# Optimization experiments

Hardware: AMD Instinct MI355X
Metric: run time of the kernel (lower is better)

The kernel has to match this reference:

```python
import jax, jax.numpy as jnp
import numpy as np

B, S, HID, NH = 2, 2048, 2048, 16
DH = HID // NH  # 128


def _rope_tables(seq_len, dim, dtype=jnp.float32):
    inv_freq = 1.0 / (10000.0 ** (jnp.arange(0, dim, 2, dtype=jnp.float32) / dim))
    t = jnp.arange(seq_len, dtype=jnp.float32)
    freqs = jnp.einsum('i,j->ij', t, inv_freq)          # [S, dim/2]
    emb = jnp.concatenate([freqs, freqs], axis=-1)       # [S, dim]
    return jnp.cos(emb)[None, None].astype(dtype), jnp.sin(emb)[None, None].astype(dtype)


def _rotate_half(x):
    x1, x2 = x[..., : x.shape[-1] // 2], x[..., x.shape[-1] // 2 :]
    return jnp.concatenate([-x2, x1], axis=-1)


def setup_inputs() -> dict:
    key = jax.random.key(0)
    ks = jax.random.split(key, 6)
    hidden_states = jax.random.normal(ks[0], (B, S, HID), dtype=jnp.float32)
    scale = 1.0 / np.sqrt(HID)
    Wq = jax.random.normal(ks[1], (HID, HID), dtype=jnp.float32) * scale
    Wk = jax.random.normal(ks[2], (HID, HID), dtype=jnp.float32) * scale
    Wv = jax.random.normal(ks[3], (HID, HID), dtype=jnp.float32) * scale
    Wo = jax.random.normal(ks[4], (HID, HID), dtype=jnp.float32) * scale
    bq = jnp.zeros((HID,), jnp.float32)
    bk = jnp.zeros((HID,), jnp.float32)
    bv = jnp.zeros((HID,), jnp.float32)
    bo = jnp.zeros((HID,), jnp.float32)
    # causal additive mask [1,1,S,S]
    causal = jnp.tril(jnp.ones((S, S), dtype=bool))
    attention_mask = jnp.where(causal, 0.0, -1e9).astype(jnp.float32)[None, None]
    return dict(hidden_states=hidden_states, attention_mask=attention_mask,
                Wq=Wq, bq=bq, Wk=Wk, bk=bk, Wv=Wv, bv=bv, Wo=Wo, bo=bo)


def reference(hidden_states, attention_mask, Wq, bq, Wk, bk, Wv, bv, Wo, bo):
    b, s, _ = hidden_states.shape
    # torch Linear: x @ W.T + b
    q = (hidden_states @ Wq.T + bq).reshape(b, s, NH, DH).transpose(0, 2, 1, 3)
    k = (hidden_states @ Wk.T + bk).reshape(b, s, NH, DH).transpose(0, 2, 1, 3)
    v = (hidden_states @ Wv.T + bv).reshape(b, s, NH, DH).transpose(0, 2, 1, 3)
    cos, sin = _rope_tables(s, DH)
    q = q * cos + _rotate_half(q) * sin
    k = k * cos + _rotate_half(k) * sin
    scores = jnp.einsum('bhqd,bhkd->bhqk', q * (DH ** -0.5), k)
    scores = scores + attention_mask
    probs = jax.nn.softmax(scores, axis=-1)  # dropout: eval mode (identity)
    out = jnp.einsum('bhqk,bhkd->bhqd', probs, v)
    out = out.transpose(0, 2, 1, 3).reshape(b, s, HID)
    return out @ Wo.T + bo
```

## Files before the change

### kernel.cpp

```cpp
#include <hip/hip_runtime.h>
#include <hip/hip_bf16.h>
#include <cstdint>
#include <cstddef>

#define BB 2
#define SS 2048
#define HH 2048
#define NHH 16
#define DHH 128

using f32x4  = __attribute__((ext_vector_type(4))) float;
using bf16x8 = __attribute__((ext_vector_type(8))) __bf16;
using bf16x4 = __attribute__((ext_vector_type(4))) __bf16;
using bfloat = __bf16;

__device__ inline void gload_lds16(const void* g, void* l) {
    __builtin_amdgcn_global_load_lds(
        (const __attribute__((address_space(1))) void*)g,
        (__attribute__((address_space(3))) void*)l, 16, 0, 0);
}

__device__ inline f32x4 mfma16(bf16x8 a, bf16x8 b, f32x4 c) {
    return __builtin_amdgcn_mfma_f32_16x16x32_bf16(a, b, c, 0, 0, 0);
}

template <int CTRL>
__device__ inline float dpp_max_step(float x) {
    int y = __builtin_amdgcn_update_dpp(0, __builtin_bit_cast(int, x), CTRL, 0xf, 0xf, false);
    return fmaxf(x, __builtin_bit_cast(float, y));
}
__device__ inline float rowmax16(float x) {
    x = dpp_max_step<0x121>(x);
    x = dpp_max_step<0x122>(x);
    x = dpp_max_step<0x124>(x);
    x = dpp_max_step<0x128>(x);
    return x;
}

__global__ void cvt_bf16(const float* __restrict__ in, bfloat* __restrict__ out, int n4) {
    int i = blockIdx.x * blockDim.x + threadIdx.x;
    if (i >= n4) return;
    float4 v = reinterpret_cast<const float4*>(in)[i];
    bf16x4 o;
    o[0] = (bfloat)v.x; o[1] = (bfloat)v.y; o[2] = (bfloat)v.z; o[3] = (bfloat)v.w;
    reinterpret_cast<bf16x4*>(out)[i] = o;
}

__global__ void cvt_bf16_w(const float* __restrict__ s0, const float* __restrict__ s1,
                           const float* __restrict__ s2, const float* __restrict__ s3,
                           bfloat* __restrict__ d0, bfloat* __restrict__ d1,
                           bfloat* __restrict__ d2, bfloat* __restrict__ d3) {
    int sel = blockIdx.x >> 12;
    int i = (blockIdx.x & 4095) * 256 + threadIdx.x;
    const float* s = sel == 0 ? s0 : sel == 1 ? s1 : sel == 2 ? s2 : s3;
    bfloat* d = sel == 0 ? d0 : sel == 1 ? d1 : sel == 2 ? d2 : d3;
    float4 v = reinterpret_cast<const float4*>(s)[i];
    bf16x4 o;
    o[0] = (bfloat)v.x; o[1] = (bfloat)v.y; o[2] = (bfloat)v.z; o[3] = (bfloat)v.w;
    reinterpret_cast<bf16x4*>(d)[i] = o;
}

__global__ void rope_table(float* __restrict__ cosT, float* __restrict__ sinT) {
    int i = blockIdx.x * blockDim.x + threadIdx.x;
    if (i >= SS * 64) return;
    int s = i >> 6, j = i & 63;
    float invf = powf(10000.0f, -(float)j / 64.0f);
    float ang = (float)s * invf;
    cosT[i] = cosf(ang);
    sinT[i] = sinf(ang);
}

__device__ __forceinline__ int cmap256(int wc, int nf) {
    return (wc >> 1) * 128 + (wc & 1) * 32 + (nf & 1) * 16 + (nf >> 1) * 64;
}

__device__ __forceinline__ void kloop256sq(const bfloat* __restrict__ Ag,
                                           const bfloat* __restrict__ Bg,
                                           f32x4 (&acc)[8][4]) {
    constexpr int K = HH, NT = K / 64;
    __shared__ bfloat Ab[2][256 * 64];
    __shared__ bfloat Bb[2][256 * 64];
    const int t = threadIdx.x, l = t & 63, lr = l & 15, lg = l >> 4;
    const int wid = t >> 6, wr = wid >> 2, wc = wid & 3;
    const int dstu = t & ~63;

    auto stage = [&](int buf, int kt) {
#pragma unroll
        for (int i = 0; i < 4; i++) {
            int U = i * 512 + t, row = U >> 3, u = (U & 7) ^ (row & 7);
            gload_lds16(Ag + (size_t)row * K + kt * 64 + u * 8,
                        &Ab[buf][(i * 512 + dstu) * 8]);
        }
#pragma unroll
        for (int i = 0; i < 4; i++) {
            int U = i * 512 + t, row = U >> 3, u = (U & 7) ^ (row & 7);
            gload_lds16(Bg + (size_t)row * K + kt * 64 + u * 8,
                        &Bb[buf][(i * 512 + dstu) * 8]);
        }
    };

    int brow[4];
#pragma unroll
    for (int nf = 0; nf < 4; nf++) brow[nf] = cmap256(wc, nf) + lr;
    const int usw[2] = { lg ^ (lr & 7), (4 + lg) ^ (lr & 7) };

    stage(0, 0);

#pragma unroll 1
    for (int kt = 0; kt < NT; ++kt) {
        const int buf = kt & 1;
        if (kt + 1 < NT) {
            stage(buf ^ 1, kt + 1);
            asm volatile("s_waitcnt vmcnt(8)" ::: "memory");
        } else {
            asm volatile("s_waitcnt vmcnt(0)" ::: "memory");
        }
        __builtin_amdgcn_s_barrier();
        __builtin_amdgcn_sched_barrier(0);

        const bfloat* A_ = Ab[buf];
        const bfloat* B_ = Bb[buf];
#pragma unroll
        for (int ks = 0; ks < 2; ++ks) {
            bf16x8 bfrag[4];
#pragma unroll
            for (int nf = 0; nf < 4; nf++)
                bfrag[nf] = *reinterpret_cast<const bf16x8*>(&B_[brow[nf] * 64 + usw[ks] * 8]);
            bf16x8 afr[4];
#pragma unroll
            for (int mf = 0; mf < 4; mf++)
                afr[mf] = *reinterpret_cast<const bf16x8*>(
                    &A_[(wr * 128 + mf * 16 + lr) * 64 + usw[ks] * 8]);
            __builtin_amdgcn_s_setprio(1);
#pragma unroll
            for (int mf = 0; mf < 4; mf++)
#pragma unroll
                for (int nf = 0; nf < 4; nf++)
                    acc[mf][nf] = mfma16(afr[mf], bfrag[nf], acc[mf][nf]);
            __builtin_amdgcn_s_setprio(0);
            __builtin_amdgcn_sched_barrier(0);
#pragma unroll
            for (int mf = 0; mf < 4; mf++)
                afr[mf] = *reinterpret_cast<const bf16x8*>(
                    &A_[(wr * 128 + (mf + 4) * 16 + lr) * 64 + usw[ks] * 8]);
            __builtin_amdgcn_s_setprio(1);
#pragma unroll
            for (int mf = 0; mf < 4; mf++)
#pragma unroll
                for (int nf = 0; nf < 4; nf++)
                    acc[mf + 4][nf] = mfma16(afr[mf], bfrag[nf], acc[mf + 4][nf]);
            __builtin_amdgcn_s_setprio(0);
            __builtin_amdgcn_sched_barrier(0);
        }
        __builtin_amdgcn_s_barrier();
    }
}

__global__ __launch_bounds__(512, 2)
void gemm_qkv(const bfloat* __restrict__ A,
              const bfloat* __restrict__ Bq, const bfloat* __restrict__ Bk,
              const bfloat* __restrict__ Bv,
              const float* __restrict__ bq, const float* __restrict__ bk,
              const float* __restrict__ bv,
              bfloat* __restrict__ Qo, bfloat* __restrict__ Ko, bfloat* __restrict__ Vto,
              const float* __restrict__ cosT, const float* __restrict__ sinT) {
    constexpr int K = HH, N = HH;
    const int sel = blockIdx.y >> 3;
    const bfloat* Bt = sel == 0 ? Bq : sel == 1 ? Bk : Bv;
    const float* bias = sel == 0 ? bq : sel == 1 ? bk : bv;
    const int m0 = blockIdx.x * 256, n0 = (blockIdx.y & 7) * 256;

    f32x4 acc[8][4] = {};
    kloop256sq(A + (size_t)m0 * K, Bt + (size_t)n0 * K, acc);

    const int t = threadIdx.x, l = t & 63, lr = l & 15, lg = l >> 4;
    const int wid = t >> 6, wr = wid >> 2, wc = wid & 3;

    if (sel == 2) {
#pragma unroll
        for (int mf = 0; mf < 8; mf++) {
            int row = m0 + wr * 128 + mf * 16 + lg * 4;
#pragma unroll
            for (int nf = 0; nf < 4; nf++) {
                int col = n0 + cmap256(wc, nf) + lr;
                float bv_ = bias[col];
#pragma unroll
                for (int j = 0; j < 4; j++) {
                    int r = row + j;
                    Vto[((size_t)((r >> 11) * HH + col)) * SS + (r & (SS - 1))] =
                        (bfloat)(acc[mf][nf][j] + bv_);
                }
            }
        }
    } else {
        bfloat* C = sel == 0 ? Qo : Ko;
        const float qs = sel == 0 ? 0.088388347648318447f : 1.0f;
        const int hbase = n0 + (wc >> 1) * 128;
#pragma unroll
        for (int mf = 0; mf < 8; mf++) {
            int row = m0 + wr * 128 + mf * 16 + lg * 4;
#pragma unroll
            for (int nf = 0; nf < 2; nf++) {
                int d = (wc & 1) * 32 + nf * 16 + lr;
                int col1 = hbase + d, col2 = col1 + 64;
                float b1 = bias[col1], b2 = bias[col2];
#pragma unroll
                for (int j = 0; j < 4; j++) {
                    int r = row + j, s = r & (SS - 1);
                    float c  = cosT[s * 64 + d];
                    float sn = sinT[s * 64 + d];
                    float x1 = acc[mf][nf][j] + b1;
                    float x2 = acc[mf][nf + 2][j] + b2;
                    C[(size_t)r * N + col1] = (bfloat)((x1 * c - x2 * sn) * qs);
                    C[(size_t)r * N + col2] = (bfloat)((x2 * c + x1 * sn) * qs);
                }
            }
        }
    }
}

__global__ __launch_bounds__(512, 2)
void gemm_out(const bfloat* __restrict__ A, const bfloat* __restrict__ Bt,
              const float* __restrict__ bias, float* __restrict__ C) {
    constexpr int K = HH, N = HH;
    const int m0 = blockIdx.x * 256, n0 = blockIdx.y * 256;

    f32x4 acc[8][4] = {};
    kloop256sq(A + (size_t)m0 * K, Bt + (size_t)n0 * K, acc);

    const int t = threadIdx.x, l = t & 63, lr = l & 15, lg = l >> 4;
    const int wid = t >> 6, wr = wid >> 2, wc = wid & 3;
#pragma unroll
    for (int mf = 0; mf < 8; mf++) {
        int row = m0 + wr * 128 + mf * 16 + lg * 4;
#pragma unroll
        for (int nf = 0; nf < 4; nf++) {
            int col = n0 + cmap256(wc, nf) + lr;
            float bv = bias[col];
#pragma unroll
            for (int j = 0; j < 4; j++)
                C[(size_t)(row + j) * N + col] = acc[mf][nf][j] + bv;
        }
    }
}

__global__ __launch_bounds__(256, 4)
void attn_fwd(const bfloat* __restrict__ Q, const bfloat* __restrict__ K,
              const bfloat* __restrict__ Vt, bfloat* __restrict__ O) {
    __shared__ bfloat Ks[64 * 128];
    __shared__ bfloat Vs[128 * 64];
    __shared__ bfloat Pw[4][16 * 64];

    const int t = threadIdx.x, w = t >> 6, l = t & 63;
    const int lr = l & 15, lg = l >> 4;
    const int swz = (lr & 7) << 4;

    const int f = blockIdx.x;
    const int xcd = f & 7, slot = f >> 3;
    const int bh = xcd + 8 * (slot >> 5);
    const int qidx = 31 - (slot & 31);
    const int b = bh >> 4, h = bh & 15;
    const int q0 = qidx * 64 + w * 16;

    const size_t bo_ = (size_t)b * SS * HH + (size_t)h * DHH;
    const bfloat* Qp = Q + bo_;
    const bfloat* Kp = K + bo_;
    const bfloat* Vp = Vt + (size_t)(b * NHH + h) * DHH * SS;
    bfloat* Op = O + bo_;

    auto stage = [&](int kv0) {
#pragma unroll
        for (int i = 0; i < 4; i++) {
            int Ub = (i * 4 + w) * 64;
            int U = Ub + l;
            int r = U >> 4;
            int u = (U & 15) ^ (r & 7);
            gload_lds16(Kp + (size_t)(kv0 + r) * HH + u * 8, &Ks[Ub * 8]);
        }
#pragma unroll
        for (int i = 0; i < 4; i++) {
            int Ub = (i * 4 + w) * 64;
            int U = Ub + l;
            int r = U >> 3;
            int u = (U & 7) ^ (r & 7);
            gload_lds16(Vp + (size_t)r * SS + kv0 + u * 8, &Vs[Ub * 8]);
        }
    };

    bf16x8 qf[4];
#pragma unroll
    for (int kt = 0; kt < 4; kt++)
        qf[kt] = *reinterpret_cast<const bf16x8*>(Qp + (size_t)(q0 + lr) * HH + kt * 32 + lg * 8);

    bf16x8 ones;
#pragma unroll
    for (int e = 0; e < 8; e++) ones[e] = (bfloat)1.0f;

    f32x4 o[8] = {};
    f32x4 lsv = {};
    float m[4];
#pragma unroll
    for (int j = 0; j < 4; j++) m[j] = -1e30f;

    const int nkv = qidx + 1;

    for (int kv = 0; kv < nkv; ++kv) {
        stage(kv * 64);
        __syncthreads();

        const char* KB = (const char*)&Ks[0];
        const char* VB = (const char*)&Vs[0];

        f32x4 sc[4] = {};
        __builtin_amdgcn_s_setprio(1);
#pragma unroll
        for (int kt = 0; kt < 4; kt++) {
            const int col = (kt * 64 + lg * 16);
#pragma unroll
            for (int kb = 0; kb < 4; kb++) {
                bf16x8 kf = *reinterpret_cast<const bf16x8*>(
                    KB + (kb * 16 + lr) * 256 + (col ^ swz));
                sc[kb] = mfma16(qf[kt], kf, sc[kb]);
            }
        }
        __builtin_amdgcn_s_setprio(0);

        const bool diag = (kv == nkv - 1);
        float p[4][4], alpha[4];
        bool ga = false;
#pragma unroll
        for (int j = 0; j < 4; j++) {
            float v0 = sc[0][j], v1 = sc[1][j], v2 = sc[2][j], v3 = sc[3][j];
            if (diag) {
                int qr = q0 + lg * 4 + j;
                int k0 = kv * 64 + lr;
                if (k0      > qr) v0 = -1e30f;
                if (k0 + 16 > qr) v1 = -1e30f;
                if (k0 + 32 > qr) v2 = -1e30f;
                if (k0 + 48 > qr) v3 = -1e30f;
            }
            float mx = rowmax16(fmaxf(fmaxf(v0, v1), fmaxf(v2, v3)));
            bool grow = mx > m[j] + 8.0f;
            float mn = grow ? mx : m[j];
            alpha[j] = grow ? __expf(m[j] - mn) : 1.0f;
            m[j] = mn;
            ga = ga || grow;
            p[0][j] = __expf(v0 - mn);
            p[1][j] = __expf(v1 - mn);
            p[2][j] = __expf(v2 - mn);
            p[3][j] = __expf(v3 - mn);
        }
        if (__any(ga)) {
#pragma unroll
            for (int j = 0; j < 4; j++) {
                lsv[j] *= alpha[j];
#pragma unroll
                for (int nt = 0; nt < 8; nt++) o[nt][j] *= alpha[j];
            }
        }

        char* pwb = (char*)&Pw[w][0];
#pragma unroll
        for (int j = 0; j < 4; j++) {
            int q = lg * 4 + j;
            int qs = (q & 7) << 4;
#pragma unroll
            for (int kb = 0; kb < 4; kb++)
                *(bfloat*)(pwb + q * 128 + ((kb * 32 + lr * 2) ^ qs)) = (bfloat)p[kb][j];
        }
        asm volatile("s_waitcnt lgkmcnt(0)" ::: "memory");
        __builtin_amdgcn_sched_barrier(0);

        const char* pwr = (const char*)&Pw[w][0];
        bf16x8 pa0 = *reinterpret_cast<const bf16x8*>(pwr + lr * 128 + ((lg * 16) ^ swz));
        bf16x8 pa1 = *reinterpret_cast<const bf16x8*>(pwr + lr * 128 + ((64 + lg * 16) ^ swz));
        __builtin_amdgcn_s_setprio(1);
        lsv = mfma16(pa0, ones, lsv);
        lsv = mfma16(pa1, ones, lsv);
#pragma unroll
        for (int nt = 0; nt < 8; nt++) {
            const char* vb = VB + (nt * 16 + lr) * 128;
            bf16x8 vf0 = *reinterpret_cast<const bf16x8*>(vb + ((lg * 16) ^ swz));
            bf16x8 vf1 = *reinterpret_cast<const bf16x8*>(vb + ((64 + lg * 16) ^ swz));
            o[nt] = mfma16(pa0, vf0, o[nt]);
            o[nt] = mfma16(pa1, vf1, o[nt]);
        }
        __builtin_amdgcn_s_setprio(0);
        __syncthreads();
    }

#pragma unroll
    for (int j = 0; j < 4; j++) {
        float inv = 1.0f / lsv[j];
        int row = q0 + lg * 4 + j;
#pragma unroll
        for (int nt = 0; nt < 8; nt++)
            Op[(size_t)row * HH + nt * 16 + lr] = (bfloat)(o[nt][j] * inv);
    }
}

extern "C" void kernel_launch(void* const* d_in, const int* in_sizes, int n_in,
                              void* d_out, int out_size, void* d_ws, size_t ws_size,
                              hipStream_t stream) {
    (void)in_sizes; (void)n_in; (void)out_size; (void)ws_size;
    const float* hs = (const float*)d_in[0];
    const float* Wq = (const float*)d_in[2];
    const float* bq = (const float*)d_in[3];
    const float* Wk = (const float*)d_in[4];
    const float* bk = (const float*)d_in[5];
    const float* Wv = (const float*)d_in[6];
    const float* bv = (const float*)d_in[7];
    const float* Wo = (const float*)d_in[8];
    const float* bo = (const float*)d_in[9];

    char* ws = (char*)d_ws;
    size_t off = 0;
    auto alloc = [&](size_t bytes) { void* p = ws + off; off += (bytes + 255) & ~(size_t)255; return p; };
    const size_t MK = (size_t)BB * SS * HH;
    const size_t NK = (size_t)HH * HH;

    bfloat* Xb  = (bfloat*)alloc(MK * 2);
    bfloat* Wqb = (bfloat*)alloc(NK * 2);
    bfloat* Wkb = (bfloat*)alloc(NK * 2);
    bfloat* Wvb = (bfloat*)alloc(NK * 2);
    bfloat* Wob = (bfloat*)alloc(NK * 2);
    bfloat* Qb  = (bfloat*)alloc(MK * 2);
    bfloat* Kb  = (bfloat*)alloc(MK * 2);
    bfloat* Vtb = (bfloat*)alloc(MK * 2);
    float*  cosT = (float*)alloc((size_t)SS * 64 * 4);
    float*  sinT = (float*)alloc((size_t)SS * 64 * 4);
    bfloat* AOb = Xb;

    cvt_bf16<<<(int)(MK / 4 / 256), 256, 0, stream>>>(hs, Xb, (int)(MK / 4));
    cvt_bf16_w<<<4 * 4096, 256, 0, stream>>>(Wq, Wk, Wv, Wo, Wqb, Wkb, Wvb, Wob);
    rope_table<<<(SS * 64 + 255) / 256, 256, 0, stream>>>(cosT, sinT);

    gemm_qkv<<<dim3(BB * SS / 256, 24), 512, 0, stream>>>(
        Xb, Wqb, Wkb, Wvb, bq, bk, bv, Qb, Kb, Vtb, cosT, sinT);

    attn_fwd<<<1024, 256, 0, stream>>>(Qb, Kb, Vtb, AOb);

    gemm_out<<<dim3(BB * SS / 256, HH / 256), 512, 0, stream>>>(
        AOb, Wob, bo, (float*)d_out);
}
```

Baseline: 329.5 us.

## Restructure GEMM k-loop into 4-phase half-tile pipeline with staggered LDS staging

Replaces the double-buffered GEMM main loop with an 8-slot scheme where A and B tiles are each split into two 128x64 halves. Each k-step runs four phases that each compute one quarter of the output. Loads for the next and the one-after-next k-tiles are issued between phases, so global-to-LDS traffic is interleaved with MFMA work rather than issued in bulk. In exchange it adds a barrier per phase and more complex waitcnt accounting, which risks extra synchronisation stalls or a race if the counts are wrong.

```diff
diff --git a/kernel.cpp b/kernel.cpp
--- a/kernel.cpp
+++ b/kernel.cpp
@@ -70,90 +70,99 @@
     sinT[i] = sinf(ang);
 }
 
-__device__ __forceinline__ int cmap256(int wc, int nf) {
-    return (wc >> 1) * 128 + (wc & 1) * 32 + (nf & 1) * 16 + (nf >> 1) * 64;
-}
-
-__device__ __forceinline__ void kloop256sq(const bfloat* __restrict__ Ag,
-                                           const bfloat* __restrict__ Bg,
-                                           f32x4 (&acc)[8][4]) {
+__device__ __forceinline__ void kloop8ph(const bfloat* __restrict__ Ag,
+                                         const bfloat* __restrict__ Bg,
+                                         f32x4 (&acc)[8][4]) {
     constexpr int K = HH, NT = K / 64;
-    __shared__ bfloat Ab[2][256 * 64];
-    __shared__ bfloat Bb[2][256 * 64];
+    __shared__ bfloat lds[2][4][128 * 64];
     const int t = threadIdx.x, l = t & 63, lr = l & 15, lg = l >> 4;
     const int wid = t >> 6, wr = wid >> 2, wc = wid & 3;
-    const int dstu = t & ~63;
-
-    auto stage = [&](int buf, int kt) {
-#pragma unroll
-        for (int i = 0; i < 4; i++) {
-            int U = i * 512 + t, row = U >> 3, u = (U & 7) ^ (row & 7);
-            gload_lds16(Ag + (size_t)row * K + kt * 64 + u * 8,
-                        &Ab[buf][(i * 512 + dstu) * 8]);
-        }
-#pragma unroll
-        for (int i = 0; i < 4; i++) {
-            int U = i * 512 + t, row = U >> 3, u = (U & 7) ^ (row & 7);
-            gload_lds16(Bg + (size_t)row * K + kt * 64 + u * 8,
-                        &Bb[buf][(i * 512 + dstu) * 8]);
+
+    auto stageSlot = [&](int buf, int slot, int kt) {
+        const bfloat* g = (slot < 2) ? Ag : Bg;
+        const int half = slot & 1;
+#pragma unroll
+        for (int i = 0; i < 2; i++) {
+            int idx = i * 512 + t;
+            int sr = idx >> 3, u = idx & 7;
+            int us = u ^ (sr & 7);
+            int grow = (sr >> 6) * 128 + half * 64 + (sr & 63);
+            gload_lds16(g + (size_t)grow * K + kt * 64 + us * 8,
+                        &lds[buf][slot][(i * 512 + (t & ~63)) * 8]);
         }
     };
 
-    int brow[4];
-#pragma unroll
-    for (int nf = 0; nf < 4; nf++) brow[nf] = cmap256(wc, nf) + lr;
-    const int usw[2] = { lg ^ (lr & 7), (4 + lg) ^ (lr & 7) };
-
-    stage(0, 0);
+    const int srA0 = wr * 64 + lr;
+    const int srB0 = (wc >> 1) * 64 + (wc & 1) * 32 + lr;
+
+    stageSlot(0, 0, 0); stageSlot(0, 1, 0); stageSlot(0, 2, 0); stageSlot(0, 3, 0);
+    stageSlot(1, 0, 1); stageSlot(1, 2, 1);
+    asm volatile("s_waitcnt vmcnt(4)" ::: "memory");
+    __builtin_amdgcn_s_barrier();
+
+    bf16x8 areg[4][2];
 
 #pragma unroll 1
     for (int kt = 0; kt < NT; ++kt) {
-        const int buf = kt & 1;
-        if (kt + 1 < NT) {
-            stage(buf ^ 1, kt + 1);
-            asm volatile("s_waitcnt vmcnt(8)" ::: "memory");
-        } else {
-            asm volatile("s_waitcnt vmcnt(0)" ::: "memory");
-        }
-        __builtin_amdgcn_s_barrier();
-        __builtin_amdgcn_sched_barrier(0);
-
-        const bfloat* A_ = Ab[buf];
-        const bfloat* B_ = Bb[buf];
-#pragma unroll
-        for (int ks = 0; ks < 2; ++ks) {
-            bf16x8 bfrag[4];
-#pragma unroll
-            for (int nf = 0; nf < 4; nf++)
-                bfrag[nf] = *reinterpret_cast<const bf16x8*>(&B_[brow[nf] * 64 + usw[ks] * 8]);
-            bf16x8 afr[4];
-#pragma unroll
-            for (int mf = 0; mf < 4; mf++)
-                afr[mf] = *reinterpret_cast<const bf16x8*>(
-                    &A_[(wr * 128 + mf * 16 + lr) * 64 + usw[ks] * 8]);
+        const int buf = kt & 1, nb = buf ^ 1;
+#pragma unroll
+        for (int ph = 0; ph < 4; ++ph) {
+            const int mh = ph >> 1, nh = ph & 1;
+            bf16x8 breg[2][2];
+#pragma unroll
+            for (int nfl = 0; nfl < 2; nfl++) {
+                int sr = srB0 + nfl * 16;
+                const bfloat* bp = &lds[buf][2 + nh][sr * 64];
+#pragma unroll
+                for (int ks = 0; ks < 2; ks++)
+                    breg[nfl][ks] = *reinterpret_cast<const bf16x8*>(
+                        bp + ((ks * 4 + lg) ^ (sr & 7)) * 8);
+            }
+            if (nh == 0) {
+#pragma unroll
+                for (int mfl = 0; mfl < 4; mfl++) {
+                    int sr = srA0 + mfl * 16;
+                    const bfloat* ap = &lds[buf][mh][sr * 64];
+#pragma unroll
+                    for (int ks = 0; ks < 2; ks++)
+                        areg[mfl][ks] = *reinterpret_cast<const bf16x8*>(
+                            ap + ((ks * 4 + lg) ^ (sr & 7)) * 8);
+                }
+            }
+            __builtin_amdgcn_sched_barrier(0);
+            if (ph == 0 && kt + 1 < NT) stageSlot(nb, 1, kt + 1);
+            if (ph == 1 && kt + 2 < NT) stageSlot(buf, 0, kt + 2);
+            if (ph == 2 && kt + 1 < NT) stageSlot(nb, 3, kt + 1);
+            if (ph == 3) {
+                if (kt + 2 < NT) {
+                    stageSlot(buf, 2, kt + 2);
+                    asm volatile("s_waitcnt vmcnt(4)" ::: "memory");
+                } else if (kt + 1 < NT) {
+                    asm volatile("s_waitcnt vmcnt(0)" ::: "memory");
+                }
+            }
+            __builtin_amdgcn_s_barrier();
+            asm volatile("s_waitcnt lgkmcnt(0)" ::: "memory");
+            __builtin_amdgcn_sched_barrier(0);
             __builtin_amdgcn_s_setprio(1);
 #pragma unroll
-            for (int mf = 0; mf < 4; mf++)
-#pragma unroll
-                for (int nf = 0; nf < 4; nf++)
-                    acc[mf][nf] = mfma16(afr[mf], bfrag[nf], acc[mf][nf]);
+            for (int ks = 0; ks < 2; ks++)
+#pragma unroll
+                for (int mfl = 0; mfl < 4; mfl++)
+#pragma unroll
+                    for (int nfl = 0; nfl < 2; nfl++)
+                        acc[mh * 4 + mfl][nh * 2 + nfl] =
+                            mfma16(areg[mfl][ks], breg[nfl][ks],
+                                   acc[mh * 4 + mfl][nh * 2 + nfl]);
             __builtin_amdgcn_s_setprio(0);
             __builtin_amdgcn_sched_barrier(0);
-#pragma unroll
-            for (int mf = 0; mf < 4; mf++)
-                afr[mf] = *reinterpret_cast<const bf16x8*>(
-                    &A_[(wr * 128 + (mf + 4) * 16 + lr) * 64 + usw[ks] * 8]);
-            __builtin_amdgcn_s_setprio(1);
-#pragma unroll
-            for (int mf = 0; mf < 4; mf++)
-#pragma unroll
-                for (int nf = 0; nf < 4; nf++)
-                    acc[mf + 4][nf] = mfma16(afr[mf], bfrag[nf], acc[mf + 4][nf]);
-            __builtin_amdgcn_s_setprio(0);
-            __builtin_amdgcn_sched_barrier(0);
-        }
-        __builtin_amdgcn_s_barrier();
+            __builtin_amdgcn_s_barrier();
+        }
     }
+}
+
+__device__ __forceinline__ int colOf(int wc, int nf, int lr) {
+    return (wc >> 1) * 128 + (nf >> 1) * 64 + (wc & 1) * 32 + (nf & 1) * 16 + lr;
 }
 
 __global__ __launch_bounds__(512, 2)
@@ -171,7 +180,7 @@
     const int m0 = blockIdx.x * 256, n0 = (blockIdx.y & 7) * 256;
 
     f32x4 acc[8][4] = {};
-    kloop256sq(A + (size_t)m0 * K, Bt + (size_t)n0 * K, acc);
+    kloop8ph(A + (size_t)m0 * K, Bt + (size_t)n0 * K, acc);
 
     const int t = threadIdx.x, l = t & 63, lr = l & 15, lg = l >> 4;
     const int wid = t >> 6, wr = wid >> 2, wc = wid & 3;
@@ -182,7 +191,7 @@
             int row = m0 + wr * 128 + mf * 16 + lg * 4;
 #pragma unroll
             for (int nf = 0; nf < 4; nf++) {
-                int col = n0 + cmap256(wc, nf) + lr;
+                int col = n0 + colOf(wc, nf, lr);
                 float bv_ = bias[col];
 #pragma unroll
                 for (int j = 0; j < 4; j++) {
@@ -226,7 +235,7 @@
     const int m0 = blockIdx.x * 256, n0 = blockIdx.y * 256;
 
     f32x4 acc[8][4] = {};
-    kloop256sq(A + (size_t)m0 * K, Bt + (size_t)n0 * K, acc);
+    kloop8ph(A + (size_t)m0 * K, Bt + (size_t)n0 * K, acc);
 
     const int t = threadIdx.x, l = t & 63, lr = l & 15, lg = l >> 4;
     const int wid = t >> 6, wr = wid >> 2, wc = wid & 3;
@@ -235,7 +244,7 @@
         int row = m0 + wr * 128 + mf * 16 + lg * 4;
 #pragma unroll
         for (int nf = 0; nf < 4; nf++) {
-            int col = n0 + cmap256(wc, nf) + lr;
+            int col = n0 + colOf(wc, nf, lr);
             float bv = bias[col];
 #pragma unroll
             for (int j = 0; j < 4; j++)
```

After: 316.2 us. 1.04x faster.
